# Optimization experiments

Measured on AMD Instinct MI355X. Metric: run time of the kernel, lower is better.

Reference implementation:

```python
import jax, jax.numpy as jnp
import numpy as np

DIM = 512
POS_DIM = 512
FROM_LEN = 4096
TO_LEN = 512
FROM_DIM = 512
TO_DIM = 512
H = 8
HD = DIM // H  # 64
B = 4
FROM_GATE_BIAS = 1.0


def setup_inputs() -> dict:
    key = jax.random.key(0)
    ks = jax.random.split(key, 24)
    s = 0.02
    d = {
        "from_tensor": jax.random.normal(ks[0], (B, FROM_LEN, FROM_DIM), jnp.float32),
        "to_tensor": jax.random.normal(ks[1], (B, TO_LEN, TO_DIM), jnp.float32),
        "from_pos": jax.random.normal(ks[2], (FROM_LEN, POS_DIM), jnp.float32),
        "to_pos": jax.random.normal(ks[3], (TO_LEN, POS_DIM), jnp.float32),
        # projection weights (torch Linear: y = x @ W + b with W stored here as [in, out])
        "Wq": jax.random.normal(ks[4], (FROM_DIM, DIM), jnp.float32) * s,
        "bq": jnp.zeros((DIM,), jnp.float32),
        "Wk": jax.random.normal(ks[5], (TO_DIM, DIM), jnp.float32) * s,
        "bk": jnp.zeros((DIM,), jnp.float32),
        "Wv": jax.random.normal(ks[6], (TO_DIM, DIM), jnp.float32) * s,
        "bv": jnp.zeros((DIM,), jnp.float32),
        "Wfp": jax.random.normal(ks[7], (POS_DIM, DIM), jnp.float32) * s,
        "bfp": jnp.zeros((DIM,), jnp.float32),
        "Wtp": jax.random.normal(ks[8], (POS_DIM, DIM), jnp.float32) * s,
        "btp": jnp.zeros((DIM,), jnp.float32),
        # to-gate (should_gate=True, from_len=1, to_len=TO_LEN, gate_bias=0)
        "Wg_to": jax.random.normal(ks[9], (DIM, H), jnp.float32) * s,
        "bg_to": jnp.zeros((H,), jnp.float32),
        "Wgp_to": jax.random.normal(ks[10], (POS_DIM, H), jnp.float32) * s,
        "bgp_to": jnp.zeros((H,), jnp.float32),
        # from-gate (should_gate=True, from_len=FROM_LEN, to_len=1, gate_bias=1)
        "Wg_from": jax.random.normal(ks[11], (DIM, H), jnp.float32) * s,
        "bg_from": jnp.zeros((H,), jnp.float32),
        "Wgp_from": jax.random.normal(ks[12], (POS_DIM, H), jnp.float32) * s,
        "bgp_from": jnp.zeros((H,), jnp.float32),
        # modulation: Linear(dim, dim) since integration='mul'
        "Wm": jax.random.normal(ks[13], (DIM, DIM), jnp.float32) * s,
        "bm": jnp.zeros((DIM,), jnp.float32),
    }
    return d


def _forward(from_tensor, to_tensor, from_pos, to_pos,
             Wq, bq, Wk, bk, Wv, bv, Wfp, bfp, Wtp, btp,
             Wg_to, bg_to, Wgp_to, bgp_to, Wg_from, bg_from, Wgp_from, bgp_from,
             Wm, bm):
    b = from_tensor.shape[0]
    f2 = from_tensor.reshape(-1, FROM_DIM)            # [B*F, from_dim]
    t2 = to_tensor.reshape(-1, TO_DIM)                # [B*T, to_dim]
    fp = jnp.tile(from_pos, (b, 1))                   # [B*F, pos_dim]
    tp = jnp.tile(to_pos, (b, 1))                     # [B*T, pos_dim]

    q = f2 @ Wq + bq + (fp @ Wfp + bfp)               # queries + from_pos_map
    k = t2 @ Wk + bk + (tp @ Wtp + btp)               # keys + to_pos_map
    v = t2 @ Wv + bv

    # transpose_for_scores -> [B, H, len, HD]
    q = q.reshape(b, FROM_LEN, H, HD).transpose(0, 2, 1, 3)
    k = k.reshape(b, TO_LEN, H, HD).transpose(0, 2, 1, 3)
    v = v.reshape(b, TO_LEN, H, HD).transpose(0, 2, 1, 3)

    scores = jnp.einsum('bhfd,bhtd->bhft', q, k) / jnp.sqrt(jnp.float32(HD))
    probs = jax.nn.softmax(scores, axis=-1)           # dropout p=0 -> identity

    # to_gate_attention: gate over to positions, broadcast over from -> [B,H,1,T]
    g_to = jax.nn.sigmoid(t2 @ Wg_to + bg_to + tp @ Wgp_to + bgp_to)
    g_to = g_to.reshape(b, 1, TO_LEN, H).transpose(0, 3, 1, 2)
    probs = probs * g_to

    # from_gate_attention (gate_bias=1): gate over from positions -> [B,H,F,1]
    g_from = jax.nn.sigmoid(f2 @ Wg_from + bg_from + fp @ Wgp_from + bgp_from + FROM_GATE_BIAS)
    g_from = g_from.reshape(b, FROM_LEN, 1, H).transpose(0, 3, 1, 2)
    probs = probs * g_from

    control = jnp.einsum('bhft,bhtd->bhfd', probs, v)   # [B,H,F,HD]
    control = control.transpose(0, 2, 1, 3).reshape(-1, DIM)  # [B*F, dim]

    # integrate: att_norm (layer norm over channels, no affine) then mul-modulation
    mu = jnp.mean(f2, axis=-1, keepdims=True)
    var = jnp.mean(jnp.square(f2 - mu), axis=-1, keepdims=True)
    tn = (f2 - mu) * jax.lax.rsqrt(var + 1e-5)
    gain = control @ Wm + bm
    out = tn * (gain + 1.0)                             # integration='mul'

    out = out.reshape(b, FROM_LEN, FROM_DIM)
    return out, probs


def reference(from_tensor, to_tensor, from_pos, to_pos,
              Wq, bq, Wk, bk, Wv, bv, Wfp, bfp, Wtp, btp,
              Wg_to, bg_to, Wgp_to, bgp_to, Wg_from, bg_from, Wgp_from, bgp_from,
              Wm, bm):
    return _forward(from_tensor, to_tensor, from_pos, to_pos,
                    Wq, bq, Wk, bk, Wv, bv, Wfp, bfp, Wtp, btp,
                    Wg_to, bg_to, Wgp_to, bgp_to, Wg_from, bg_from, Wgp_from, bgp_from,
                    Wm, bm)
```

## Files before the change

kernel.cpp:

```cpp
#include <hip/hip_runtime.h>
#include <hip/hip_bf16.h>
#include <stdint.h>

#define FLEN 4096
#define TLEN 512
#define NB   4
#define NH   8

typedef __attribute__((ext_vector_type(8))) short short8;
typedef __attribute__((ext_vector_type(4))) float floatx4;
typedef unsigned short ushort_t;
typedef unsigned int uint_t;

typedef __attribute__((address_space(1))) const void gconst_as;
typedef __attribute__((address_space(3))) void lds_as;

__device__ inline ushort_t f2bf(float f) {
    union { float f; uint_t u; } v; v.f = f;
    uint_t r = (v.u + 0x7FFFu + ((v.u >> 16) & 1u)) >> 16;
    return (ushort_t)r;
}
__device__ inline float bf2f(uint_t u) {
    union { uint_t u; float f; } v; v.u = u << 16;
    return v.f;
}
__device__ inline short8 pack_bf16(floatx4 a, floatx4 b) {
    short8 r;
    r[0]=(short)f2bf(a[0]); r[1]=(short)f2bf(a[1]); r[2]=(short)f2bf(a[2]); r[3]=(short)f2bf(a[3]);
    r[4]=(short)f2bf(b[0]); r[5]=(short)f2bf(b[1]); r[6]=(short)f2bf(b[2]); r[7]=(short)f2bf(b[3]);
    return r;
}

__global__ __launch_bounds__(256) void conv_from_stats(const float* __restrict__ X,
                                                       ushort_t* __restrict__ Xb,
                                                       float* __restrict__ S) {
    int w = threadIdx.x >> 6, l = threadIdx.x & 63;
    int row = blockIdx.x * 4 + w;
    const float* xr = X + (size_t)row * 512;
    floatx4 v0 = *(const floatx4*)(xr + l * 8);
    floatx4 v1 = *(const floatx4*)(xr + l * 8 + 4);
    *(short8*)(Xb + (size_t)row * 512 + l * 8) = pack_bf16(v0, v1);
    float s = 0.f, q = 0.f;
    #pragma unroll
    for (int j = 0; j < 4; ++j) { s += v0[j] + v1[j]; q += v0[j]*v0[j] + v1[j]*v1[j]; }
    #pragma unroll
    for (int off = 1; off < 64; off <<= 1) { s += __shfl_xor(s, off); q += __shfl_xor(q, off); }
    if (l == 0) {
        float mu = s * (1.f / 512.f);
        float var = q * (1.f / 512.f) - mu * mu;
        S[row * 2] = mu;
        S[row * 2 + 1] = rsqrtf(var + 1e-5f);
    }
}

__global__ void conv3(const float* __restrict__ to, ushort_t* __restrict__ tob,
                      const float* __restrict__ fpos, ushort_t* __restrict__ fposb,
                      const float* __restrict__ tpos, ushort_t* __restrict__ tposb) {
    int bid = blockIdx.x;
    const float* src; ushort_t* dst; int i;
    if (bid < 512)       { src = to;   dst = tob;   i = bid * 256 + threadIdx.x; }
    else if (bid < 1536) { src = fpos; dst = fposb; i = (bid - 512) * 256 + threadIdx.x; }
    else                 { src = tpos; dst = tposb; i = (bid - 1536) * 256 + threadIdx.x; }
    floatx4 v0 = *(const floatx4*)(src + (size_t)i * 8);
    floatx4 v1 = *(const floatx4*)(src + (size_t)i * 8 + 4);
    *(short8*)(dst + (size_t)i * 8) = pack_bf16(v0, v1);
}

struct T6Args {
    const float* s[6];
    ushort_t* d[6];
    int stride[6];
    int coff[6];
};
__global__ __launch_bounds__(256) void transpose6(T6Args a) {
    int m = blockIdx.x >> 6;
    int bx = blockIdx.x & 7, by = (blockIdx.x >> 3) & 7;
    __shared__ float tile[64][65];
    int rb = by * 64, cb = bx * 64;
    int tr = threadIdx.x >> 6, tc = threadIdx.x & 63;
    const float* src = a.s[m];
    #pragma unroll
    for (int i = 0; i < 16; ++i) {
        int rr = tr + i * 4;
        tile[rr][tc] = src[(size_t)(rb + rr) * 512 + cb + tc];
    }
    __syncthreads();
    ushort_t* dst = a.d[m];
    int stride = a.stride[m], coff = a.coff[m];
    #pragma unroll
    for (int i = 0; i < 16; ++i) {
        int rr = tr + i * 4;
        dst[(size_t)(cb + rr) * stride + coff + rb + tc] = f2bf(tile[tc][rr]);
    }
}

__global__ void prep(const float* bq, const float* bfp, const float* bk, const float* btp,
                     const float* bgF, const float* bgpF, const float* bgT, const float* bgpT,
                     const float* WgF, const float* WgpF, const float* WgT_, const float* WgpT,
                     float* bqf, float* bkt, float* bgFc, float* bgTc,
                     ushort_t* WgFT, ushort_t* WgTT) {
    int i = blockIdx.x * 256 + threadIdx.x;
    if (i < 512) { bqf[i] = bq[i] + bfp[i]; bkt[i] = bk[i] + btp[i]; }
    if (i < 8) { bgFc[i] = bgF[i] + bgpF[i] + 1.0f; bgTc[i] = bgT[i] + bgpT[i]; }
    int j = i >> 10, k = i & 1023;
    float vF = 0.f, vT = 0.f;
    if (j < 8) {
        vF = (k < 512) ? WgF[k * 8 + j] : WgpF[(k - 512) * 8 + j];
        vT = (k < 512) ? WgT_[k * 8 + j] : WgpT[(k - 512) * 8 + j];
    }
    WgFT[i] = f2bf(vF);
    WgTT[i] = f2bf(vT);
}

__global__ __launch_bounds__(256, 2) void gemm_bf16(
    const ushort_t* __restrict__ A1, const ushort_t* __restrict__ A2, int rm, int K,
    const ushort_t* __restrict__ WT, const float* __restrict__ bias,
    float* __restrict__ Cf, ushort_t* __restrict__ Cb,
    const float* __restrict__ f2, const float* __restrict__ stats, int epi)
{
    __shared__ ushort_t As[128 * 64];
    __shared__ ushort_t Bs[128 * 64];
    int tid = threadIdx.x;
    int w = tid >> 6, l = tid & 63, fr = l & 15, g = l >> 4;
    int wr = w >> 1, wc = w & 1;
    int rb = blockIdx.x * 128, cb = blockIdx.y * 128;

    floatx4 acc[4][4];
    #pragma unroll
    for (int mt = 0; mt < 4; ++mt)
        #pragma unroll
        for (int nt = 0; nt < 4; ++nt)
            #pragma unroll
            for (int i = 0; i < 4; ++i) acc[mt][nt][i] = 0.f;

    int srow = w * 8 + (l >> 3);
    int scx = ((l & 7) ^ (l >> 3)) * 8;

    for (int kb = 0; kb < K; kb += 64) {
        #pragma unroll
        for (int i = 0; i < 4; ++i) {
            int ra = rb + i * 32 + srow;
            int ka = kb + scx;
            const ushort_t* ga = (ka < 512) ? (A1 + (size_t)ra * 512 + ka)
                                            : (A2 + (size_t)(ra & rm) * 512 + (ka - 512));
            __builtin_amdgcn_global_load_lds((gconst_as*)ga, (lds_as*)(As + i * 2048 + w * 512), 16, 0, 0);
            const ushort_t* gb = WT + (size_t)(cb + i * 32 + srow) * K + kb + scx;
            __builtin_amdgcn_global_load_lds((gconst_as*)gb, (lds_as*)(Bs + i * 2048 + w * 512), 16, 0, 0);
        }
        __syncthreads();
        #pragma unroll
        for (int kk = 0; kk < 2; ++kk) {
            int co = (kk * 32 + g * 8) ^ ((fr & 7) * 8);
            short8 af[4], bw[4];
            #pragma unroll
            for (int mt = 0; mt < 4; ++mt)
                af[mt] = *(const short8*)&As[(wr * 64 + mt * 16 + fr) * 64 + co];
            #pragma unroll
            for (int nt = 0; nt < 4; ++nt)
                bw[nt] = *(const short8*)&Bs[(wc * 64 + nt * 16 + fr) * 64 + co];
            #pragma unroll
            for (int mt = 0; mt < 4; ++mt)
                #pragma unroll
                for (int nt = 0; nt < 4; ++nt)
                    acc[mt][nt] = __builtin_amdgcn_mfma_f32_16x16x32_bf16(af[mt], bw[nt], acc[mt][nt], 0, 0, 0);
        }
        __syncthreads();
    }

    #pragma unroll
    for (int mt = 0; mt < 4; ++mt) {
        #pragma unroll
        for (int nt = 0; nt < 4; ++nt) {
            #pragma unroll
            for (int i = 0; i < 4; ++i) {
                int r = rb + wr * 64 + mt * 16 + g * 4 + i;
                int c = cb + wc * 64 + nt * 16 + fr;
                float v = acc[mt][nt][i];
                if (epi == 0) {
                    Cb[(size_t)r * 512 + c] = f2bf(v + bias[c]);
                } else if (epi == 2) {
                    int bb = r >> 9, t = r & 511, hh = c >> 6, d = c & 63;
                    size_t idx = ((size_t)((bb * 8 + hh) * 64 + d)) * 512 +
                                 (t & ~31) + ((t >> 2) & 3) * 8 + ((t >> 4) & 1) * 4 + (t & 3);
                    Cb[idx] = f2bf(v + bias[c]);
                } else {
                    float mu = stats[r * 2], rs = stats[r * 2 + 1];
                    Cf[(size_t)r * 512 + c] = (f2[(size_t)r * 512 + c] - mu) * rs * (v + bias[c] + 1.0f);
                }
            }
        }
    }
}

__global__ __launch_bounds__(256) void gate_mfma(
    const ushort_t* __restrict__ A1, const ushort_t* __restrict__ A2, int rm,
    const ushort_t* __restrict__ WgT, const float* __restrict__ bgc,
    float* __restrict__ G, int layout)
{
    int tid = threadIdx.x, w = tid >> 6, l = tid & 63;
    int fr = l & 15, g = l >> 4;
    int rb = blockIdx.x * 64 + w * 16;
    int arow = rb + fr;
    floatx4 acc = {0.f, 0.f, 0.f, 0.f};
    #pragma unroll
    for (int ks = 0; ks < 32; ++ks) {
        int k0 = ks * 32 + g * 8;
        const ushort_t* ap = (k0 < 512) ? (A1 + (size_t)arow * 512 + k0)
                                        : (A2 + (size_t)(arow & rm) * 512 + (k0 - 512));
        short8 af = *(const short8*)ap;
        short8 bw = *(const short8*)(WgT + (size_t)fr * 1024 + k0);
        acc = __builtin_amdgcn_mfma_f32_16x16x32_bf16(af, bw, acc, 0, 0, 0);
    }
    if (fr < 8) {
        #pragma unroll
        for (int i = 0; i < 4; ++i) {
            int r = rb + g * 4 + i;
            float z = acc[i] + bgc[fr];
            float gv = 1.f / (1.f + __expf(-z));
            if (layout == 0) G[((size_t)((r >> 12) * 8 + fr)) * FLEN + (r & 4095)] = gv;
            else G[((size_t)((r >> 9) * 8 + fr)) * 512 + (r & 511)] = gv;
        }
    }
}

__global__ __launch_bounds__(256, 2) void attn_kernel(
    const ushort_t* __restrict__ Q, const ushort_t* __restrict__ K,
    const ushort_t* __restrict__ Vp,
    const float* __restrict__ gFromT, const float* __restrict__ gToT,
    float* __restrict__ probs, ushort_t* __restrict__ ctrl)
{
    __shared__ float chunkbuf[4][16 * 132];
    int tid = threadIdx.x, w = tid >> 6, l = tid & 63;
    int fr = l & 15, g = l >> 4;
    int bh = blockIdx.y, b = bh >> 3, h = bh & 7;
    int fb = blockIdx.x * 64 + w * 16;
    int f = fb + fr;

    const ushort_t* qp = Q + ((size_t)(b * FLEN) + f) * 512 + h * 64 + g * 8;
    short8 qf0 = *(const short8*)qp;
    short8 qf1 = *(const short8*)(qp + 32);

    uint_t pbx[32], pby[32];
    float ssum = 0.f;
    const float* gtp = gToT + (size_t)bh * 512;

    #pragma unroll
    for (int tt = 0; tt < 32; ++tt) {
        const ushort_t* kp = K + ((size_t)(b * TLEN) + tt * 16 + fr) * 512 + h * 64 + g * 8;
        short8 kf0 = *(const short8*)kp;
        short8 kf1 = *(const short8*)(kp + 32);
        floatx4 sc = {0.f, 0.f, 0.f, 0.f};
        sc = __builtin_amdgcn_mfma_f32_16x16x32_bf16(kf0, qf0, sc, 0, 0, 0);
        sc = __builtin_amdgcn_mfma_f32_16x16x32_bf16(kf1, qf1, sc, 0, 0, 0);
        floatx4 gt = *(const floatx4*)(gtp + tt * 16 + g * 4);
        float e0 = __expf(sc[0] * 0.125f), e1 = __expf(sc[1] * 0.125f);
        float e2 = __expf(sc[2] * 0.125f), e3 = __expf(sc[3] * 0.125f);
        ssum += e0 + e1 + e2 + e3;
        float p0 = e0 * gt[0], p1 = e1 * gt[1], p2 = e2 * gt[2], p3 = e3 * gt[3];
        pbx[tt] = (uint_t)f2bf(p0) | ((uint_t)f2bf(p1) << 16);
        pby[tt] = (uint_t)f2bf(p2) | ((uint_t)f2bf(p3) << 16);
    }
    ssum += __shfl_xor(ssum, 16);
    ssum += __shfl_xor(ssum, 32);
    float fac = gFromT[(size_t)bh * FLEN + f] / ssum;

    floatx4 oacc[4];
    #pragma unroll
    for (int dt = 0; dt < 4; ++dt)
        #pragma unroll
        for (int i = 0; i < 4; ++i) oacc[dt][i] = 0.f;

    #pragma unroll
    for (int kt = 0; kt < 16; ++kt) {
        union { uint_t u[4]; short8 v; } bu;
        bu.u[0] = pbx[2 * kt];     bu.u[1] = pby[2 * kt];
        bu.u[2] = pbx[2 * kt + 1]; bu.u[3] = pby[2 * kt + 1];
        #pragma unroll
        for (int dt = 0; dt < 4; ++dt) {
            const ushort_t* vp = Vp + ((size_t)(bh * 64) + dt * 16 + fr) * 512 + kt * 32 + g * 8;
            short8 vf = *(const short8*)vp;
            oacc[dt] = __builtin_amdgcn_mfma_f32_16x16x32_bf16(vf, bu.v, oacc[dt], 0, 0, 0);
        }
    }

    float* cbuf = chunkbuf[w];
    int il2 = l >> 5, pos = l & 31;
    #pragma unroll
    for (int c = 0; c < 4; ++c) {
        #pragma unroll
        for (int t8 = 0; t8 < 8; ++t8) {
            int tt = c * 8 + t8;
            floatx4 pv;
            pv[0] = bf2f(pbx[tt] & 0xffffu) * fac;
            pv[1] = bf2f(pbx[tt] >> 16) * fac;
            pv[2] = bf2f(pby[tt] & 0xffffu) * fac;
            pv[3] = bf2f(pby[tt] >> 16) * fac;
            *(floatx4*)&cbuf[fr * 132 + t8 * 16 + g * 4] = pv;
        }
        #pragma unroll
        for (int rr = 0; rr < 8; ++rr) {
            int row = rr * 2 + il2;
            *(floatx4*)(probs + ((size_t)bh * FLEN + fb + row) * 512 + c * 128 + pos * 4)
                = *(const floatx4*)&cbuf[row * 132 + pos * 4];
        }
    }

    ushort_t* ctile = (ushort_t*)cbuf;
    #pragma unroll
    for (int dt = 0; dt < 4; ++dt)
        #pragma unroll
        for (int i = 0; i < 4; ++i)
            ctile[fr * 72 + dt * 16 + g * 4 + i] = f2bf(oacc[dt][i] * fac);

    int fl = l >> 2, dp = (l & 3) * 16;
    uint4 c0 = *(const uint4*)&ctile[fl * 72 + dp];
    uint4 c1 = *(const uint4*)&ctile[fl * 72 + dp + 8];
    ushort_t* cdst = ctrl + ((size_t)(b * FLEN) + fb + fl) * 512 + h * 64 + dp;
    *(uint4*)cdst = c0;
    *(uint4*)(cdst + 8) = c1;
}

extern "C" void kernel_launch(void* const* d_in, const int* in_sizes, int n_in,
                              void* d_out, int out_size, void* d_ws, size_t ws_size,
                              hipStream_t stream) {
    const float* from = (const float*)d_in[0];
    const float* to   = (const float*)d_in[1];
    const float* fpos = (const float*)d_in[2];
    const float* tpos = (const float*)d_in[3];
    const float* Wq  = (const float*)d_in[4];  const float* bq  = (const float*)d_in[5];
    const float* Wk  = (const float*)d_in[6];  const float* bk  = (const float*)d_in[7];
    const float* Wv  = (const float*)d_in[8];  const float* bv  = (const float*)d_in[9];
    const float* Wfp = (const float*)d_in[10]; const float* bfp = (const float*)d_in[11];
    const float* Wtp = (const float*)d_in[12]; const float* btp = (const float*)d_in[13];
    const float* Wg_to   = (const float*)d_in[14]; const float* bg_to   = (const float*)d_in[15];
    const float* Wgp_to  = (const float*)d_in[16]; const float* bgp_to  = (const float*)d_in[17];
    const float* Wg_from = (const float*)d_in[18]; const float* bg_from = (const float*)d_in[19];
    const float* Wgp_from= (const float*)d_in[20]; const float* bgp_from= (const float*)d_in[21];
    const float* Wm  = (const float*)d_in[22]; const float* bm  = (const float*)d_in[23];

    char* ws = (char*)d_ws;
    ushort_t* WqfT = (ushort_t*)ws; ws += 512 * 1024 * 2;
    ushort_t* WktT = (ushort_t*)ws; ws += 512 * 1024 * 2;
    ushort_t* WvT  = (ushort_t*)ws; ws += 512 * 512 * 2;
    ushort_t* WmT  = (ushort_t*)ws; ws += 512 * 512 * 2;
    ushort_t* WgFT = (ushort_t*)ws; ws += 16 * 1024 * 2;
    ushort_t* WgTT = (ushort_t*)ws; ws += 16 * 1024 * 2;
    float* bqf  = (float*)ws; ws += 512 * 4;
    float* bkt  = (float*)ws; ws += 512 * 4;
    float* bgFc = (float*)ws; ws += 64 * 4;
    float* bgTc = (float*)ws; ws += 64 * 4;
    ushort_t* fbf = (ushort_t*)ws; ws += (size_t)NB * FLEN * 512 * 2;
    ushort_t* tbf = (ushort_t*)ws; ws += (size_t)NB * TLEN * 512 * 2;
    ushort_t* Qbf = (ushort_t*)ws; ws += (size_t)NB * FLEN * 512 * 2;
    ushort_t* Kbf = (ushort_t*)ws; ws += (size_t)NB * TLEN * 512 * 2;
    ushort_t* Vp  = (ushort_t*)ws; ws += (size_t)NB * NH * 64 * 512 * 2;
    float* gFromT = (float*)ws; ws += (size_t)NB * NH * FLEN * 4;
    float* gToT   = (float*)ws; ws += (size_t)NB * NH * 512 * 4;
    ushort_t* ctrl = (ushort_t*)ws; ws += (size_t)NB * FLEN * 512 * 2;
    float* stats = (float*)ws; ws += (size_t)NB * FLEN * 2 * 4;
    if (ws_size < (size_t)(ws - (char*)d_ws)) return;
    ushort_t* fposbf = ctrl;
    ushort_t* tposbf = ctrl + (size_t)FLEN * 512;

    conv_from_stats<<<NB * FLEN / 4, 256, 0, stream>>>(from, fbf, stats);
    conv3<<<1664, 256, 0, stream>>>(to, tbf, fpos, fposbf, tpos, tposbf);

    T6Args ta;
    ta.s[0] = Wq;  ta.d[0] = WqfT; ta.stride[0] = 1024; ta.coff[0] = 0;
    ta.s[1] = Wfp; ta.d[1] = WqfT; ta.stride[1] = 1024; ta.coff[1] = 512;
    ta.s[2] = Wk;  ta.d[2] = WktT; ta.stride[2] = 1024; ta.coff[2] = 0;
    ta.s[3] = Wtp; ta.d[3] = WktT; ta.stride[3] = 1024; ta.coff[3] = 512;
    ta.s[4] = Wv;  ta.d[4] = WvT;  ta.stride[4] = 512;  ta.coff[4] = 0;
    ta.s[5] = Wm;  ta.d[5] = WmT;  ta.stride[5] = 512;  ta.coff[5] = 0;
    transpose6<<<384, 256, 0, stream>>>(ta);

    prep<<<64, 256, 0, stream>>>(bq, bfp, bk, btp,
                                 bg_from, bgp_from, bg_to, bgp_to,
                                 Wg_from, Wgp_from, Wg_to, Wgp_to,
                                 bqf, bkt, bgFc, bgTc, WgFT, WgTT);

    gemm_bf16<<<dim3(NB * FLEN / 128, 4), 256, 0, stream>>>(fbf, fposbf, FLEN - 1, 1024, WqfT, bqf, nullptr, Qbf, nullptr, nullptr, 0);
    gemm_bf16<<<dim3(NB * TLEN / 128, 4), 256, 0, stream>>>(tbf, tposbf, TLEN - 1, 1024, WktT, bkt, nullptr, Kbf, nullptr, nullptr, 0);
    gemm_bf16<<<dim3(NB * TLEN / 128, 4), 256, 0, stream>>>(tbf, tbf, TLEN - 1, 512, WvT, bv, nullptr, Vp, nullptr, nullptr, 2);

    gate_mfma<<<NB * FLEN / 64, 256, 0, stream>>>(fbf, fposbf, FLEN - 1, WgFT, bgFc, gFromT, 0);
    gate_mfma<<<NB * TLEN / 64, 256, 0, stream>>>(tbf, tposbf, TLEN - 1, WgTT, bgTc, gToT, 1);

    float* out = (float*)d_out;
    attn_kernel<<<dim3(FLEN / 64, NB * NH), 256, 0, stream>>>(Qbf, Kbf, Vp, gFromT, gToT,
                                                              out + (size_t)NB * FLEN * 512, ctrl);

    gemm_bf16<<<dim3(NB * FLEN / 128, 4), 256, 0, stream>>>(ctrl, ctrl, FLEN - 1, 512, WmT, bm, out, nullptr, from, stats, 3);
}
```

Measured before the change: 627.6 us.

## Recompute attention scores in a second pass to drop register arrays and raise occupancy

The attention kernel no longer keeps all 32 tiles of bf16 probabilities in registers. A first pass now computes only the softmax denominator, and a second pass recomputes QK^T per chunk, feeding P·V and streaming the probs output through a smaller LDS buffer. With fewer registers and less shared memory, launch bounds rise from 2 to 4 blocks per SM, trading doubled QK MFMA work and K reloads for more parallelism. The two fp32-to-bf16 conversion kernels are also merged into one launch.

```diff
diff --git a/kernel.cpp b/kernel.cpp
--- a/kernel.cpp
+++ b/kernel.cpp
@@ -31,32 +31,34 @@
     return r;
 }
 
-__global__ __launch_bounds__(256) void conv_from_stats(const float* __restrict__ X,
-                                                       ushort_t* __restrict__ Xb,
-                                                       float* __restrict__ S) {
-    int w = threadIdx.x >> 6, l = threadIdx.x & 63;
-    int row = blockIdx.x * 4 + w;
-    const float* xr = X + (size_t)row * 512;
-    floatx4 v0 = *(const floatx4*)(xr + l * 8);
-    floatx4 v1 = *(const floatx4*)(xr + l * 8 + 4);
-    *(short8*)(Xb + (size_t)row * 512 + l * 8) = pack_bf16(v0, v1);
-    float s = 0.f, q = 0.f;
-    #pragma unroll
-    for (int j = 0; j < 4; ++j) { s += v0[j] + v1[j]; q += v0[j]*v0[j] + v1[j]*v1[j]; }
-    #pragma unroll
-    for (int off = 1; off < 64; off <<= 1) { s += __shfl_xor(s, off); q += __shfl_xor(q, off); }
-    if (l == 0) {
-        float mu = s * (1.f / 512.f);
-        float var = q * (1.f / 512.f) - mu * mu;
-        S[row * 2] = mu;
-        S[row * 2 + 1] = rsqrtf(var + 1e-5f);
-    }
-}
-
-__global__ void conv3(const float* __restrict__ to, ushort_t* __restrict__ tob,
-                      const float* __restrict__ fpos, ushort_t* __restrict__ fposb,
-                      const float* __restrict__ tpos, ushort_t* __restrict__ tposb) {
+__global__ __launch_bounds__(256) void conv_all(
+    const float* __restrict__ from, ushort_t* __restrict__ fbf, float* __restrict__ S,
+    const float* __restrict__ to, ushort_t* __restrict__ tob,
+    const float* __restrict__ fpos, ushort_t* __restrict__ fposb,
+    const float* __restrict__ tpos, ushort_t* __restrict__ tposb)
+{
     int bid = blockIdx.x;
+    if (bid < 4096) {
+        int w = threadIdx.x >> 6, l = threadIdx.x & 63;
+        int row = bid * 4 + w;
+        const float* xr = from + (size_t)row * 512;
+        floatx4 v0 = *(const floatx4*)(xr + l * 8);
+        floatx4 v1 = *(const floatx4*)(xr + l * 8 + 4);
+        *(short8*)(fbf + (size_t)row * 512 + l * 8) = pack_bf16(v0, v1);
+        float s = 0.f, q = 0.f;
+        #pragma unroll
+        for (int j = 0; j < 4; ++j) { s += v0[j] + v1[j]; q += v0[j]*v0[j] + v1[j]*v1[j]; }
+        #pragma unroll
+        for (int off = 1; off < 64; off <<= 1) { s += __shfl_xor(s, off); q += __shfl_xor(q, off); }
+        if (l == 0) {
+            float mu = s * (1.f / 512.f);
+            float var = q * (1.f / 512.f) - mu * mu;
+            S[row * 2] = mu;
+            S[row * 2 + 1] = rsqrtf(var + 1e-5f);
+        }
+        return;
+    }
+    bid -= 4096;
     const float* src; ushort_t* dst; int i;
     if (bid < 512)       { src = to;   dst = tob;   i = bid * 256 + threadIdx.x; }
     else if (bid < 1536) { src = fpos; dst = fposb; i = (bid - 512) * 256 + threadIdx.x; }
@@ -223,13 +225,13 @@
     }
 }
 
-__global__ __launch_bounds__(256, 2) void attn_kernel(
+__global__ __launch_bounds__(256, 4) void attn_kernel(
     const ushort_t* __restrict__ Q, const ushort_t* __restrict__ K,
     const ushort_t* __restrict__ Vp,
     const float* __restrict__ gFromT, const float* __restrict__ gToT,
     float* __restrict__ probs, ushort_t* __restrict__ ctrl)
 {
-    __shared__ float chunkbuf[4][16 * 132];
+    __shared__ float chunkbuf[4][16 * 68];
     int tid = threadIdx.x, w = tid >> 6, l = tid & 63;
     int fr = l & 15, g = l >> 4;
     int bh = blockIdx.y, b = bh >> 3, h = bh & 7;
@@ -239,31 +241,27 @@
     const ushort_t* qp = Q + ((size_t)(b * FLEN) + f) * 512 + h * 64 + g * 8;
     short8 qf0 = *(const short8*)qp;
     short8 qf1 = *(const short8*)(qp + 32);
-
-    uint_t pbx[32], pby[32];
+    const ushort_t* kbase = K + (size_t)(b * TLEN) * 512 + h * 64;
+
     float ssum = 0.f;
-    const float* gtp = gToT + (size_t)bh * 512;
-
     #pragma unroll
     for (int tt = 0; tt < 32; ++tt) {
-        const ushort_t* kp = K + ((size_t)(b * TLEN) + tt * 16 + fr) * 512 + h * 64 + g * 8;
+        const ushort_t* kp = kbase + (size_t)(tt * 16 + fr) * 512 + g * 8;
         short8 kf0 = *(const short8*)kp;
         short8 kf1 = *(const short8*)(kp + 32);
         floatx4 sc = {0.f, 0.f, 0.f, 0.f};
         sc = __builtin_amdgcn_mfma_f32_16x16x32_bf16(kf0, qf0, sc, 0, 0, 0);
         sc = __builtin_amdgcn_mfma_f32_16x16x32_bf16(kf1, qf1, sc, 0, 0, 0);
-        floatx4 gt = *(const floatx4*)(gtp + tt * 16 + g * 4);
-        float e0 = __expf(sc[0] * 0.125f), e1 = __expf(sc[1] * 0.125f);
-        float e2 = __expf(sc[2] * 0.125f), e3 = __expf(sc[3] * 0.125f);
-        ssum += e0 + e1 + e2 + e3;
-        float p0 = e0 * gt[0], p1 = e1 * gt[1], p2 = e2 * gt[2], p3 = e3 * gt[3];
-        pbx[tt] = (uint_t)f2bf(p0) | ((uint_t)f2bf(p1) << 16);
-        pby[tt] = (uint_t)f2bf(p2) | ((uint_t)f2bf(p3) << 16);
+        ssum += __expf(sc[0] * 0.125f) + __expf(sc[1] * 0.125f)
+              + __expf(sc[2] * 0.125f) + __expf(sc[3] * 0.125f);
     }
     ssum += __shfl_xor(ssum, 16);
     ssum += __shfl_xor(ssum, 32);
     float fac = gFromT[(size_t)bh * FLEN + f] / ssum;
 
+    const float* gtp = gToT + (size_t)bh * 512;
+    float* cbuf = chunkbuf[w];
+    size_t pbase = ((size_t)bh * FLEN + fb) * 512;
     floatx4 oacc[4];
     #pragma unroll
     for (int dt = 0; dt < 4; ++dt)
@@ -271,37 +269,44 @@
         for (int i = 0; i < 4; ++i) oacc[dt][i] = 0.f;
 
     #pragma unroll
-    for (int kt = 0; kt < 16; ++kt) {
-        union { uint_t u[4]; short8 v; } bu;
-        bu.u[0] = pbx[2 * kt];     bu.u[1] = pby[2 * kt];
-        bu.u[2] = pbx[2 * kt + 1]; bu.u[3] = pby[2 * kt + 1];
-        #pragma unroll
-        for (int dt = 0; dt < 4; ++dt) {
-            const ushort_t* vp = Vp + ((size_t)(bh * 64) + dt * 16 + fr) * 512 + kt * 32 + g * 8;
-            short8 vf = *(const short8*)vp;
-            oacc[dt] = __builtin_amdgcn_mfma_f32_16x16x32_bf16(vf, bu.v, oacc[dt], 0, 0, 0);
-        }
-    }
-
-    float* cbuf = chunkbuf[w];
-    int il2 = l >> 5, pos = l & 31;
-    #pragma unroll
-    for (int c = 0; c < 4; ++c) {
-        #pragma unroll
-        for (int t8 = 0; t8 < 8; ++t8) {
-            int tt = c * 8 + t8;
-            floatx4 pv;
-            pv[0] = bf2f(pbx[tt] & 0xffffu) * fac;
-            pv[1] = bf2f(pbx[tt] >> 16) * fac;
-            pv[2] = bf2f(pby[tt] & 0xffffu) * fac;
-            pv[3] = bf2f(pby[tt] >> 16) * fac;
-            *(floatx4*)&cbuf[fr * 132 + t8 * 16 + g * 4] = pv;
-        }
-        #pragma unroll
-        for (int rr = 0; rr < 8; ++rr) {
-            int row = rr * 2 + il2;
-            *(floatx4*)(probs + ((size_t)bh * FLEN + fb + row) * 512 + c * 128 + pos * 4)
-                = *(const floatx4*)&cbuf[row * 132 + pos * 4];
+    for (int c = 0; c < 8; ++c) {
+        uint_t px[4], py[4];
+        #pragma unroll
+        for (int j = 0; j < 4; ++j) {
+            int tt = c * 4 + j;
+            const ushort_t* kp = kbase + (size_t)(tt * 16 + fr) * 512 + g * 8;
+            short8 kf0 = *(const short8*)kp;
+            short8 kf1 = *(const short8*)(kp + 32);
+            floatx4 sc = {0.f, 0.f, 0.f, 0.f};
+            sc = __builtin_amdgcn_mfma_f32_16x16x32_bf16(kf0, qf0, sc, 0, 0, 0);
+            sc = __builtin_amdgcn_mfma_f32_16x16x32_bf16(kf1, qf1, sc, 0, 0, 0);
+            floatx4 gt = *(const floatx4*)(gtp + tt * 16 + g * 4);
+            float e0 = __expf(sc[0] * 0.125f), e1 = __expf(sc[1] * 0.125f);
+            float e2 = __expf(sc[2] * 0.125f), e3 = __expf(sc[3] * 0.125f);
+            float p0 = e0 * gt[0], p1 = e1 * gt[1], p2 = e2 * gt[2], p3 = e3 * gt[3];
+            px[j] = (uint_t)f2bf(p0) | ((uint_t)f2bf(p1) << 16);
+            py[j] = (uint_t)f2bf(p2) | ((uint_t)f2bf(p3) << 16);
+            floatx4 pv = { p0 * fac, p1 * fac, p2 * fac, p3 * fac };
+            *(floatx4*)&cbuf[fr * 68 + j * 16 + g * 4] = pv;
+        }
+        #pragma unroll
+        for (int kk = 0; kk < 2; ++kk) {
+            union { uint_t u[4]; short8 v; } bu;
+            bu.u[0] = px[2 * kk];     bu.u[1] = py[2 * kk];
+            bu.u[2] = px[2 * kk + 1]; bu.u[3] = py[2 * kk + 1];
+            int kt = c * 2 + kk;
+            #pragma unroll
+            for (int dt = 0; dt < 4; ++dt) {
+                const ushort_t* vp = Vp + ((size_t)(bh * 64) + dt * 16 + fr) * 512 + kt * 32 + g * 8;
+                short8 vf = *(const short8*)vp;
+                oacc[dt] = __builtin_amdgcn_mfma_f32_16x16x32_bf16(vf, bu.v, oacc[dt], 0, 0, 0);
+            }
+        }
+        #pragma unroll
+        for (int rr = 0; rr < 4; ++rr) {
+            int row = rr * 4 + g;
+            *(floatx4*)(probs + pbase + (size_t)row * 512 + c * 64 + fr * 4)
+                = *(const floatx4*)&cbuf[row * 68 + fr * 4];
         }
     }
 
@@ -362,8 +367,7 @@
     ushort_t* fposbf = ctrl;
     ushort_t* tposbf = ctrl + (size_t)FLEN * 512;
 
-    conv_from_stats<<<NB * FLEN / 4, 256, 0, stream>>>(from, fbf, stats);
-    conv3<<<1664, 256, 0, stream>>>(to, tbf, fpos, fposbf, tpos, tposbf);
+    conv_all<<<5760, 256, 0, stream>>>(from, fbf, stats, to, tbf, fpos, fposbf, tpos, tposbf);
 
     T6Args ta;
     ta.s[0] = Wq;  ta.d[0] = WqfT; ta.stride[0] = 1024; ta.coff[0] = 0;
```

New measurement: 660.5 us. +5.3%, slower.
